# Optimization experiments

Hardware: AMD Instinct MI355X
Metric: run time of the kernel (lower is better)

## Reference

```python
import jax, jax.numpy as jnp
import numpy as np

N = 100000   # nodes
E = 640000   # edges
D = 128      # feature dim
G = 512      # graphs in the batch


def setup_inputs() -> dict:
    key = jax.random.key(0)
    ks = jax.random.split(key, 6)
    x = jax.random.normal(ks[0], (N, D), dtype=jnp.float32)
    edge_index = jax.random.randint(ks[1], (2, E), 0, N, dtype=jnp.int32)
    batch = jnp.sort(jax.random.randint(ks[2], (N,), 0, G, dtype=jnp.int32))
    scale = 1.0 / np.sqrt(D)
    W0 = jax.random.normal(ks[3], (D, D), dtype=jnp.float32) * scale
    W1 = jax.random.normal(ks[4], (D, D), dtype=jnp.float32) * scale
    W2 = jax.random.normal(ks[5], (D, D), dtype=jnp.float32) * scale
    return {"x": x, "edge_index": edge_index, "batch": batch,
            "W0": W0, "W1": W1, "W2": W2}


def gcn_conv(x, W, row, col, n):
    """GCNConv (bias=False): x' = D^-1/2 (A + I) D^-1/2 (x @ W).
    row/col already include self-loops."""
    xw = x @ W                                              # [N, D]
    deg = jax.ops.segment_sum(jnp.ones_like(col, dtype=x.dtype), col,
                              num_segments=n)               # [N]
    dinv = jnp.where(deg > 0, jax.lax.rsqrt(deg), 0.0)
    norm = dinv[row] * dinv[col]                            # [E+N]
    msgs = norm[:, None] * xw[row]                          # gather + scale
    return jax.ops.segment_sum(msgs, col, num_segments=n)   # scatter-add


def reference(x, edge_index, batch, W0, W1, W2):
    n = x.shape[0]
    loops = jnp.arange(n, dtype=edge_index.dtype)
    row = jnp.concatenate([edge_index[0], loops])
    col = jnp.concatenate([edge_index[1], loops])
    # conv_layers[:-1] (no activation between them in forward)
    x = gcn_conv(x, W0, row, col, n)
    x = gcn_conv(x, W1, row, col, n)
    x = jax.nn.leaky_relu(x, negative_slope=0.01)
    x = gcn_conv(x, W2, row, col, n)
    # global_add_pool over graph ids
    return jax.ops.segment_sum(x, batch, num_segments=G)    # [G, D]
```

## Files before the change

### kernel.cpp

```cpp
#include <hip/hip_runtime.h>
#include <hip/hip_bf16.h>

#define FEAT 128

typedef unsigned int uint32;
typedef unsigned short ushort16;
typedef __attribute__((ext_vector_type(8))) short short8;
typedef __attribute__((ext_vector_type(4))) float v4f;
typedef __attribute__((ext_vector_type(2))) float f32x2;

__device__ __forceinline__ ushort16 f2bf(float f) {
    uint32 u = __float_as_uint(f);
    u += 0x7fffu + ((u >> 16) & 1u);
    return (ushort16)(u >> 16);
}
__device__ __forceinline__ float bflo(uint32 u) { return __uint_as_float(u << 16); }
__device__ __forceinline__ float bfhi(uint32 u) { return __uint_as_float(u & 0xffff0000u); }
__device__ __forceinline__ f32x2 up2(uint32 u) { return (f32x2){bflo(u), bfhi(u)}; }

__device__ __forceinline__ void gemm_body(const float* __restrict__ A,
                                          const ushort16* __restrict__ Wt,
                                          ushort16* __restrict__ Ch, int n,
                                          int pairId, int pairStride,
                                          int tile0, int tile1, int t) {
    const int w = t >> 6;
    const int lane = t & 63;
    const int quad = lane >> 4;
    const int l16 = lane & 15;
    const int colBase = (w & 1) * 64;

    short8 wf[4][4];
#pragma unroll
    for (int ct = 0; ct < 4; ct++) {
        const ushort16* wp = Wt + (size_t)(colBase + ct * 16 + l16) * FEAT + quad * 8;
#pragma unroll
        for (int ks = 0; ks < 4; ks++) wf[ct][ks] = *(const short8*)(wp + ks * 32);
    }

    int tile = tile0 + pairId;
    if (tile >= tile1) return;

    auto loadA = [&](int tl, short8 (&a)[4]) {
        const int rowi = tl * 16 + l16;
        if (rowi < n) {
#pragma unroll
            for (int ks = 0; ks < 4; ks++) {
                const float* ap = A + (size_t)rowi * FEAT + quad * 8 + ks * 32;
                float4 f0 = *(const float4*)ap;
                float4 f1 = *(const float4*)(ap + 4);
                short8 v;
                v[0] = f2bf(f0.x); v[1] = f2bf(f0.y); v[2] = f2bf(f0.z); v[3] = f2bf(f0.w);
                v[4] = f2bf(f1.x); v[5] = f2bf(f1.y); v[6] = f2bf(f1.z); v[7] = f2bf(f1.w);
                a[ks] = v;
            }
        } else {
#pragma unroll
            for (int ks = 0; ks < 4; ks++) a[ks] = (short8)0;
        }
    };

    short8 aCur[4];
    loadA(tile, aCur);

    while (tile < tile1) {
        const int nextTile = tile + pairStride;
        short8 aNxt[4];
        if (nextTile < tile1) loadA(nextTile, aNxt);

        v4f acc[4];
#pragma unroll
        for (int ct = 0; ct < 4; ct++) acc[ct] = (v4f)0.f;
#pragma unroll
        for (int ct = 0; ct < 4; ct++)
#pragma unroll
            for (int ks = 0; ks < 4; ks++)
                acc[ct] = __builtin_amdgcn_mfma_f32_16x16x32_bf16(wf[ct][ks], aCur[ks], acc[ct], 0, 0, 0);

        const int rowi = tile * 16 + l16;
        if (rowi < n) {
#pragma unroll
            for (int ct = 0; ct < 4; ct++) {
                uint2 o;
                o.x = (uint32)f2bf(acc[ct][0]) | ((uint32)f2bf(acc[ct][1]) << 16);
                o.y = (uint32)f2bf(acc[ct][2]) | ((uint32)f2bf(acc[ct][3]) << 16);
                *(uint2*)(Ch + (size_t)rowi * FEAT + colBase + ct * 16 + quad * 4) = o;
            }
        }

        tile = nextTile;
#pragma unroll
        for (int ks = 0; ks < 4; ks++) aCur[ks] = aNxt[ks];
    }
}

__global__ __launch_bounds__(256) void pre_kernel(int* __restrict__ counts, int n,
                                                  const float* __restrict__ W0,
                                                  const float* __restrict__ W1,
                                                  ushort16* __restrict__ W01t,
                                                  float* __restrict__ Pbuf) {
    int b = blockIdx.x;
    int t = threadIdx.x;
    if (b < 100) {
        int idx = (b * 256 + t) * 4;
        if (idx + 3 < n) {
            *(int4*)(counts + idx) = make_int4(0, 0, 0, 0);
        } else {
            for (int i = idx; i < n; i++) counts[i] = 0;
        }
    } else if (b < 164) {
        __shared__ float sW0[2][FEAT];
        int wb = b - 100;
        int lk = t >> 7;
        int ncol = t & 127;
        int k = wb * 2 + lk;
        sW0[lk][ncol] = W0[(size_t)k * FEAT + ncol];
        __syncthreads();
        float acc = 0.f;
#pragma unroll 4
        for (int j = 0; j < FEAT; j++)
            acc += sW0[lk][j] * W1[(size_t)j * FEAT + ncol];
        W01t[(size_t)ncol * FEAT + k] = f2bf(acc);
    } else {
        int zb = b - 164;
        float4 z = make_float4(0.f, 0.f, 0.f, 0.f);
        float* p = Pbuf + (size_t)zb * 2048 + t * 8;
        *(float4*)p = z;
        *(float4*)(p + 4) = z;
    }
}

__global__ __launch_bounds__(256) void histgemmA_kernel(const int* __restrict__ col,
                                                        int* __restrict__ counts, int E,
                                                        const float* __restrict__ A,
                                                        const ushort16* __restrict__ Wt,
                                                        ushort16* __restrict__ Ch, int n) {
    const int b = blockIdx.x;
    const int r9 = b % 9;
    const int g9 = b / 9;
    const int t = threadIdx.x;
    if (r9 >= 4) {
        int hb = g9 * 5 + (r9 - 4);
        int id = hb * 256 + t;
        if (id * 4 + 3 < E) {
            int4 c4 = *(const int4*)(col + id * 4);
            atomicAdd(&counts[c4.x], 1);
            atomicAdd(&counts[c4.y], 1);
            atomicAdd(&counts[c4.z], 1);
            atomicAdd(&counts[c4.w], 1);
        } else {
            for (int e = id * 4; e < E; e++) atomicAdd(&counts[col[e]], 1);
        }
        return;
    }
    int gb = g9 * 4 + r9;
    gemm_body(A, Wt, Ch, n, gb * 2 + ((t >> 6) >> 1), 1024, 0, 3125, t);
}

__global__ __launch_bounds__(256) void scan_part(const int* __restrict__ counts,
                                                 int* __restrict__ bsum, int n) {
    __shared__ int s[256];
    int base = blockIdx.x * 1024;
    int t = threadIdx.x;
    int v = 0;
#pragma unroll
    for (int i = 0; i < 4; i++) {
        int idx = base + t * 4 + i;
        if (idx < n) v += counts[idx];
    }
    s[t] = v;
    __syncthreads();
    for (int o = 128; o > 0; o >>= 1) {
        if (t < o) s[t] += s[t + o];
        __syncthreads();
    }
    if (t == 0) bsum[blockIdx.x] = s[0];
}

__global__ __launch_bounds__(256) void scan_final(const int* __restrict__ counts,
                                                  const int* __restrict__ bsum,
                                                  int* __restrict__ off, int* __restrict__ nxt,
                                                  float* __restrict__ dinv, int n, int nb) {
    __shared__ int s[256];
    __shared__ int sb[128];
    int base = blockIdx.x * 1024;
    int t = threadIdx.x;
    if (t < nb) sb[t] = bsum[t];
    int c[4];
    int sum = 0;
#pragma unroll
    for (int i = 0; i < 4; i++) {
        int idx = base + t * 4 + i;
        c[i] = (idx < n) ? counts[idx] : 0;
        sum += c[i];
    }
    int v0 = sum;
    s[t] = sum;
    __syncthreads();
    for (int o = 1; o < 256; o <<= 1) {
        int v = (t >= o) ? s[t - o] : 0;
        __syncthreads();
        s[t] += v;
        __syncthreads();
    }
    int blockBase = 0;
    for (int j = 0; j < blockIdx.x; j++) blockBase += sb[j];
    int excl = s[t] - v0 + blockBase;
#pragma unroll
    for (int i = 0; i < 4; i++) {
        int idx = base + t * 4 + i;
        if (idx < n) {
            off[idx] = excl;
            nxt[idx] = excl;
            dinv[idx] = rsqrtf((float)(c[i] + 1));
        }
        excl += c[i];
    }
    if (blockIdx.x == gridDim.x - 1 && t == 255) off[n] = excl;
}

__global__ __launch_bounds__(256) void fillgemmB_kernel(const float* __restrict__ A,
                                                        const ushort16* __restrict__ Wt,
                                                        ushort16* __restrict__ Ch, int n,
                                                        const int* __restrict__ row,
                                                        const int* __restrict__ col,
                                                        int* __restrict__ nxt,
                                                        int* __restrict__ srcArr, int E) {
    const int b = blockIdx.x;
    const int r7 = b % 7;
    const int g7 = b / 7;
    const int t = threadIdx.x;
    if (r7 >= 2) {
        int fb = g7 * 5 + (r7 - 2);
        int e = fb * 256 + t;
        if (e < E) {
            int c = col[e], r = row[e];
            int p = atomicAdd(&nxt[c], 1);
            __builtin_nontemporal_store(r, &srcArr[p]);
        }
        return;
    }
    int gb = g7 * 2 + r7;
    gemm_body(A, Wt, Ch, n, gb * 2 + ((t >> 6) >> 1), 2048, 3125, 6250, t);
}

__global__ __launch_bounds__(256) void gather_kernel(const int* __restrict__ off,
                                                     const int* __restrict__ srcArr,
                                                     const float* __restrict__ dinv,
                                                     const ushort16* __restrict__ XWh,
                                                     ushort16* __restrict__ Hh, int n,
                                                     int leaky) {
    int node = blockIdx.x * 4 + (threadIdx.x >> 6);
    if (node >= n) return;
    int lane = threadIdx.x & 63;
    int grp = lane >> 4;
    int l16 = lane & 15;
    float dc = dinv[node];
    const uint4* table = (const uint4*)XWh;

    f32x2 acc[4];
    if (grp == 0) {
        uint4 v = table[(size_t)node * 16 + l16];
        f32x2 w0 = (f32x2){dc * dc, dc * dc};
        acc[0] = w0 * up2(v.x);
        acc[1] = w0 * up2(v.y);
        acc[2] = w0 * up2(v.z);
        acc[3] = w0 * up2(v.w);
    } else {
#pragma unroll
        for (int j = 0; j < 4; j++) acc[j] = (f32x2){0.f, 0.f};
    }

    int s = off[node], e = off[node + 1];
    int i = s + grp;
    for (; i + 4 < e; i += 8) {
        int r0 = srcArr[i];
        int r1 = srcArr[i + 4];
        uint4 u0 = table[(size_t)r0 * 16 + l16];
        uint4 u1 = table[(size_t)r1 * 16 + l16];
        float f0 = dc * dinv[r0];
        float f1 = dc * dinv[r1];
        f32x2 n0 = (f32x2){f0, f0};
        f32x2 n1 = (f32x2){f1, f1};
        acc[0] += n0 * up2(u0.x);
        acc[1] += n0 * up2(u0.y);
        acc[2] += n0 * up2(u0.z);
        acc[3] += n0 * up2(u0.w);
        acc[0] += n1 * up2(u1.x);
        acc[1] += n1 * up2(u1.y);
        acc[2] += n1 * up2(u1.z);
        acc[3] += n1 * up2(u1.w);
    }
    if (i < e) {
        int r0 = srcArr[i];
        uint4 u0 = table[(size_t)r0 * 16 + l16];
        float f0 = dc * dinv[r0];
        f32x2 n0 = (f32x2){f0, f0};
        acc[0] += n0 * up2(u0.x);
        acc[1] += n0 * up2(u0.y);
        acc[2] += n0 * up2(u0.z);
        acc[3] += n0 * up2(u0.w);
    }

    float b[8] = {acc[0].x, acc[0].y, acc[1].x, acc[1].y,
                  acc[2].x, acc[2].y, acc[3].x, acc[3].y};
#pragma unroll
    for (int j = 0; j < 8; j++) {
        b[j] += __shfl_xor(b[j], 16);
        b[j] += __shfl_xor(b[j], 32);
    }

    if (grp == 0) {
        if (leaky) {
#pragma unroll
            for (int j = 0; j < 8; j++) b[j] = (b[j] >= 0.f) ? b[j] : 0.01f * b[j];
        }
        uint4 o;
        o.x = (uint32)f2bf(b[0]) | ((uint32)f2bf(b[1]) << 16);
        o.y = (uint32)f2bf(b[2]) | ((uint32)f2bf(b[3]) << 16);
        o.z = (uint32)f2bf(b[4]) | ((uint32)f2bf(b[5]) << 16);
        o.w = (uint32)f2bf(b[6]) | ((uint32)f2bf(b[7]) << 16);
        *(uint4*)(Hh + (size_t)node * FEAT + l16 * 8) = o;
    }
}

__global__ __launch_bounds__(128) void pool_kernel(const ushort16* __restrict__ H,
                                                   const int* __restrict__ batch,
                                                   float* __restrict__ P, int n) {
    int t = threadIdx.x;
    int i0 = blockIdx.x * 32;
    if (i0 >= n) return;
    int i1 = min(i0 + 32, n);
    float acc = 0.f;
    int g = batch[i0];
    for (int i = i0; i < i1; i++) {
        int b = batch[i];
        if (b != g) {
            atomicAdd(&P[(size_t)g * FEAT + t], acc);
            acc = 0.f;
            g = b;
        }
        uint32 u = (uint32)(unsigned short)H[(size_t)i * FEAT + t];
        acc += __uint_as_float(u << 16);
    }
    atomicAdd(&P[(size_t)g * FEAT + t], acc);
}

__global__ __launch_bounds__(128) void pgemm_kernel(const float* __restrict__ P,
                                                    const float* __restrict__ W2,
                                                    float* __restrict__ out) {
    __shared__ float sP[FEAT];
    const int g = blockIdx.x;
    const int t = threadIdx.x;
    sP[t] = P[(size_t)g * FEAT + t];
    __syncthreads();
    float o = 0.f;
#pragma unroll 4
    for (int k = 0; k < FEAT; k++) o += sP[k] * W2[(size_t)k * FEAT + t];
    out[(size_t)g * FEAT + t] = o;
}

extern "C" void kernel_launch(void* const* d_in, const int* in_sizes, int n_in,
                              void* d_out, int out_size, void* d_ws, size_t ws_size,
                              hipStream_t stream) {
    const float* x = (const float*)d_in[0];
    const int* ei = (const int*)d_in[1];
    const int* batch = (const int*)d_in[2];
    const float* W0 = (const float*)d_in[3];
    const float* W1 = (const float*)d_in[4];
    const float* W2 = (const float*)d_in[5];
    float* out = (float*)d_out;

    const int N = in_sizes[0] / FEAT;
    const int E = in_sizes[1] / 2;
    const int G = out_size / FEAT;

    const int* rowI = ei;
    const int* colI = ei + E;

    char* ws = (char*)d_ws;
    auto take = [&](size_t bytes) {
        char* p = ws;
        ws += (bytes + 15) & ~(size_t)15;
        return p;
    };
    int* counts    = (int*)take((size_t)N * 4);
    int* off       = (int*)take((size_t)(N + 1) * 4);
    int* nxt       = (int*)take((size_t)N * 4);
    float* dinv    = (float*)take((size_t)N * 4);
    int* bsum      = (int*)take(128 * 4);
    int* srcArr    = (int*)take((size_t)E * 4);
    ushort16* W01t = (ushort16*)take((size_t)16384 * 2);
    float* Pbuf    = (float*)take((size_t)G * FEAT * 4);
    ushort16* bufA = (ushort16*)take((size_t)N * FEAT * 2);
    ushort16* bufB = (ushort16*)take((size_t)N * FEAT * 2);

    const int nb = (N + 1023) / 1024;

    pre_kernel<<<196, 256, 0, stream>>>(counts, N, W0, W1, W01t, Pbuf);

    histgemmA_kernel<<<128 * 9, 256, 0, stream>>>(colI, counts, E, x, W01t, bufA, N);

    scan_part<<<nb, 256, 0, stream>>>(counts, bsum, N);
    scan_final<<<nb, 256, 0, stream>>>(counts, bsum, off, nxt, dinv, N, nb);

    fillgemmB_kernel<<<512 * 7, 256, 0, stream>>>(x, W01t, bufA, N,
                                                  rowI, colI, nxt, srcArr, E);

    const int gatBlocks = (N + 3) / 4;
    gather_kernel<<<gatBlocks, 256, 0, stream>>>(off, srcArr, dinv, bufA, bufB, N, 0);
    gather_kernel<<<gatBlocks, 256, 0, stream>>>(off, srcArr, dinv, bufB, bufA, N, 1);
    gather_kernel<<<gatBlocks, 256, 0, stream>>>(off, srcArr, dinv, bufA, bufB, N, 0);
    pool_kernel<<<(N + 31) / 32, 128, 0, stream>>>(bufB, batch, Pbuf, N);
    pgemm_kernel<<<G, 128, 0, stream>>>(Pbuf, W2, out);
}
```

Measured before the change: 332.1 us.

## Fuse final gather with pooling and overlap GEMM tiles with scan

The last gather kernel now pools directly. Each block stages its four node rows in shared memory and atomically adds per-graph partial sums into the pool buffer, so the third bf16 hidden buffer is never written and the separate pool kernel is gone. The GEMM tile range is also re-split so that some tiles run in extra blocks of the scan_final kernel, hiding that small serial kernel behind useful work. In exchange there are many more global atomics on the pooled output (one per feature per block, up to 25k blocks), and the load balance across the three GEMM-carrying kernels changes.

```diff
diff --git a/kernel.cpp b/kernel.cpp
--- a/kernel.cpp
+++ b/kernel.cpp
@@ -153,7 +153,7 @@
         return;
     }
     int gb = g9 * 4 + r9;
-    gemm_body(A, Wt, Ch, n, gb * 2 + ((t >> 6) >> 1), 1024, 0, 3125, t);
+    gemm_body(A, Wt, Ch, n, gb * 2 + ((t >> 6) >> 1), 1024, 0, 1750, t);
 }
 
 __global__ __launch_bounds__(256) void scan_part(const int* __restrict__ counts,
@@ -176,14 +176,22 @@
     if (t == 0) bsum[blockIdx.x] = s[0];
 }
 
-__global__ __launch_bounds__(256) void scan_final(const int* __restrict__ counts,
-                                                  const int* __restrict__ bsum,
-                                                  int* __restrict__ off, int* __restrict__ nxt,
-                                                  float* __restrict__ dinv, int n, int nb) {
+__global__ __launch_bounds__(256) void scanfinalgemm_kernel(
+        const int* __restrict__ counts, const int* __restrict__ bsum,
+        int* __restrict__ off, int* __restrict__ nxt,
+        float* __restrict__ dinv, int n, int nb,
+        const float* __restrict__ A, const ushort16* __restrict__ Wt,
+        ushort16* __restrict__ Ch) {
+    const int b = blockIdx.x;
+    const int t = threadIdx.x;
+    if (b >= nb) {
+        int gb = b - nb;
+        gemm_body(A, Wt, Ch, n, gb * 2 + ((t >> 6) >> 1), 768, 1750, 2500, t);
+        return;
+    }
     __shared__ int s[256];
     __shared__ int sb[128];
-    int base = blockIdx.x * 1024;
-    int t = threadIdx.x;
+    int base = b * 1024;
     if (t < nb) sb[t] = bsum[t];
     int c[4];
     int sum = 0;
@@ -203,7 +211,7 @@
         __syncthreads();
     }
     int blockBase = 0;
-    for (int j = 0; j < blockIdx.x; j++) blockBase += sb[j];
+    for (int j = 0; j < b; j++) blockBase += sb[j];
     int excl = s[t] - v0 + blockBase;
 #pragma unroll
     for (int i = 0; i < 4; i++) {
@@ -215,7 +223,7 @@
         }
         excl += c[i];
     }
-    if (blockIdx.x == gridDim.x - 1 && t == 255) off[n] = excl;
+    if (b == nb - 1 && t == 255) off[n] = excl;
 }
 
 __global__ __launch_bounds__(256) void fillgemmB_kernel(const float* __restrict__ A,
@@ -240,22 +248,17 @@
         return;
     }
     int gb = g7 * 2 + r7;
-    gemm_body(A, Wt, Ch, n, gb * 2 + ((t >> 6) >> 1), 2048, 3125, 6250, t);
-}
-
-__global__ __launch_bounds__(256) void gather_kernel(const int* __restrict__ off,
-                                                     const int* __restrict__ srcArr,
-                                                     const float* __restrict__ dinv,
-                                                     const ushort16* __restrict__ XWh,
-                                                     ushort16* __restrict__ Hh, int n,
-                                                     int leaky) {
-    int node = blockIdx.x * 4 + (threadIdx.x >> 6);
-    if (node >= n) return;
-    int lane = threadIdx.x & 63;
+    gemm_body(A, Wt, Ch, n, gb * 2 + ((t >> 6) >> 1), 2048, 2500, 6250, t);
+}
+
+__device__ __forceinline__ void gather_body(const int* __restrict__ off,
+                                            const int* __restrict__ srcArr,
+                                            const float* __restrict__ dinv,
+                                            const uint4* __restrict__ table,
+                                            int node, int lane, float* b) {
     int grp = lane >> 4;
     int l16 = lane & 15;
     float dc = dinv[node];
-    const uint4* table = (const uint4*)XWh;
 
     f32x2 acc[4];
     if (grp == 0) {
@@ -301,19 +304,32 @@
         acc[3] += n0 * up2(u0.w);
     }
 
-    float b[8] = {acc[0].x, acc[0].y, acc[1].x, acc[1].y,
-                  acc[2].x, acc[2].y, acc[3].x, acc[3].y};
+    b[0] = acc[0].x; b[1] = acc[0].y; b[2] = acc[1].x; b[3] = acc[1].y;
+    b[4] = acc[2].x; b[5] = acc[2].y; b[6] = acc[3].x; b[7] = acc[3].y;
 #pragma unroll
     for (int j = 0; j < 8; j++) {
         b[j] += __shfl_xor(b[j], 16);
         b[j] += __shfl_xor(b[j], 32);
     }
-
-    if (grp == 0) {
+}
+
+__global__ __launch_bounds__(256) void gather_kernel(const int* __restrict__ off,
+                                                     const int* __restrict__ srcArr,
+                                                     const float* __restrict__ dinv,
+                                                     const ushort16* __restrict__ XWh,
+                                                     ushort16* __restrict__ Hh, int n,
+                                                     int leaky) {
+    int node = blockIdx.x * 4 + (threadIdx.x >> 6);
+    if (node >= n) return;
+    int lane = threadIdx.x & 63;
+    float b[8];
+    gather_body(off, srcArr, dinv, (const uint4*)XWh, node, lane, b);
+    if ((lane >> 4) == 0) {
         if (leaky) {
 #pragma unroll
             for (int j = 0; j < 8; j++) b[j] = (b[j] >= 0.f) ? b[j] : 0.01f * b[j];
         }
+        int l16 = lane & 15;
         uint4 o;
         o.x = (uint32)f2bf(b[0]) | ((uint32)f2bf(b[1]) << 16);
         o.y = (uint32)f2bf(b[2]) | ((uint32)f2bf(b[3]) << 16);
@@ -323,26 +339,50 @@
     }
 }
 
-__global__ __launch_bounds__(128) void pool_kernel(const ushort16* __restrict__ H,
-                                                   const int* __restrict__ batch,
-                                                   float* __restrict__ P, int n) {
-    int t = threadIdx.x;
-    int i0 = blockIdx.x * 32;
-    if (i0 >= n) return;
-    int i1 = min(i0 + 32, n);
-    float acc = 0.f;
-    int g = batch[i0];
-    for (int i = i0; i < i1; i++) {
-        int b = batch[i];
-        if (b != g) {
-            atomicAdd(&P[(size_t)g * FEAT + t], acc);
-            acc = 0.f;
-            g = b;
-        }
-        uint32 u = (uint32)(unsigned short)H[(size_t)i * FEAT + t];
-        acc += __uint_as_float(u << 16);
-    }
-    atomicAdd(&P[(size_t)g * FEAT + t], acc);
+__global__ __launch_bounds__(256) void gatherpool_kernel(const int* __restrict__ off,
+                                                         const int* __restrict__ srcArr,
+                                                         const float* __restrict__ dinv,
+                                                         const ushort16* __restrict__ XWh,
+                                                         const int* __restrict__ batch,
+                                                         float* __restrict__ Pbuf, int n) {
+    __shared__ float sH[4][FEAT];
+    __shared__ int sG[4];
+    const int w = threadIdx.x >> 6;
+    const int node = blockIdx.x * 4 + w;
+    const int lane = threadIdx.x & 63;
+    const bool valid = node < n;
+
+    float b[8];
+    if (valid) {
+        gather_body(off, srcArr, dinv, (const uint4*)XWh, node, lane, b);
+        if (lane == 0) sG[w] = batch[node];
+        if ((lane >> 4) == 0) {
+            int l16 = lane & 15;
+#pragma unroll
+            for (int k = 0; k < 8; k++) sH[w][l16 * 8 + k] = b[k];
+        }
+    } else if (lane == 0) {
+        sG[w] = -1;
+    }
+    __syncthreads();
+
+    if (threadIdx.x < FEAT) {
+        int f = threadIdx.x;
+        float acc = 0.f;
+        int g = -1;
+#pragma unroll
+        for (int ww = 0; ww < 4; ww++) {
+            int gw = sG[ww];
+            if (gw < 0) continue;
+            if (gw != g) {
+                if (g >= 0) atomicAdd(&Pbuf[(size_t)g * FEAT + f], acc);
+                acc = 0.f;
+                g = gw;
+            }
+            acc += sH[ww][f];
+        }
+        if (g >= 0) atomicAdd(&Pbuf[(size_t)g * FEAT + f], acc);
+    }
 }
 
 __global__ __launch_bounds__(128) void pgemm_kernel(const float* __restrict__ P,
@@ -401,7 +441,9 @@
     histgemmA_kernel<<<128 * 9, 256, 0, stream>>>(colI, counts, E, x, W01t, bufA, N);
 
     scan_part<<<nb, 256, 0, stream>>>(counts, bsum, N);
-    scan_final<<<nb, 256, 0, stream>>>(counts, bsum, off, nxt, dinv, N, nb);
+
+    scanfinalgemm_kernel<<<nb + 384, 256, 0, stream>>>(counts, bsum, off, nxt, dinv,
+                                                       N, nb, x, W01t, bufA);
 
     fillgemmB_kernel<<<512 * 7, 256, 0, stream>>>(x, W01t, bufA, N,
                                                   rowI, colI, nxt, srcArr, E);
@@ -409,7 +451,6 @@
     const int gatBlocks = (N + 3) / 4;
     gather_kernel<<<gatBlocks, 256, 0, stream>>>(off, srcArr, dinv, bufA, bufB, N, 0);
     gather_kernel<<<gatBlocks, 256, 0, stream>>>(off, srcArr, dinv, bufB, bufA, N, 1);
-    gather_kernel<<<gatBlocks, 256, 0, stream>>>(off, srcArr, dinv, bufA, bufB, N, 0);
-    pool_kernel<<<(N + 31) / 32, 128, 0, stream>>>(bufB, batch, Pbuf, N);
+    gatherpool_kernel<<<gatBlocks, 256, 0, stream>>>(off, srcArr, dinv, bufA, batch, Pbuf, N);
     pgemm_kernel<<<G, 128, 0, stream>>>(Pbuf, W2, out);
 }
```

Result: no change. 337.7 us (+1.7%).
